# Kernel tuning notes

Measured on AMD Instinct MI355X. Metric: run time of the kernel, lower is better.

Reference implementation:

```python
import jax, jax.numpy as jnp
import numpy as np

BATCH, SEQ = 2, 4096
IN_FEATURES = 4096
OUT_FEATURES = 4096
BLOCK = 64                      # oft_block_size (bs)
RANK = IN_FEATURES // BLOCK     # number of diagonal blocks (r)


def setup_inputs() -> dict:
    key = jax.random.key(0)
    k1, k2, k3, k4 = jax.random.split(key, 4)
    x = jax.random.normal(k1, (BATCH, SEQ, IN_FEATURES), dtype=jnp.float32)
    # OFT adapter parameters: one (bs x bs) generator per block
    oft_r = jax.random.normal(k2, (RANK, BLOCK, BLOCK), dtype=jnp.float32) * 0.02
    # Dequantized GPTQ weight (out_features x in_features) + bias
    W = jax.random.normal(k3, (OUT_FEATURES, IN_FEATURES), dtype=jnp.float32) * 0.02
    b = jax.random.normal(k4, (OUT_FEATURES,), dtype=jnp.float32)
    return {"x": x, "oft_r": oft_r, "W": W, "b": b}


def _cayley_batch(data):
    # data: [r, bs, bs].  Q = (I - skew) @ (I + skew)^{-1}  (torch.linalg.solve left=False)
    bs = data.shape[-1]
    skew = 0.5 * (data - jnp.swapaxes(data, -1, -2))
    I = jnp.eye(bs, dtype=data.dtype)
    A = I + skew   # [r, bs, bs]
    B = I - skew
    # Solve Q A = B  ->  A^T Q^T = B^T
    Qt = jnp.linalg.solve(jnp.swapaxes(A, -1, -2), jnp.swapaxes(B, -1, -2))
    return jnp.swapaxes(Qt, -1, -2)


def reference(x, oft_r, W, b):
    rank, bs, _ = oft_r.shape
    # oft_rotation starts as identity; single active adapter -> rotation = Cayley(oft_r)
    oft_rotation = _cayley_batch(oft_r)            # [rank, bs, bs]
    batch_dims = x.shape[:-1]
    x_reshaped = x.reshape(*batch_dims, rank, bs)  # [..., r, k]
    x_rot = jnp.einsum('...rk,rkc->...rc', x_reshaped, oft_rotation)
    x_rot = x_rot.reshape(*batch_dims, rank * bs)  # [..., in_features]
    # quant_linear_module (dequantized): y = x_rot @ W^T + b
    return jnp.einsum('bsi,oi->bso', x_rot, W) + b
```

## Files before the change

### kernel.cpp

```cpp
#include <hip/hip_runtime.h>
#include <hip/hip_bf16.h>
#include <stdint.h>


typedef __bf16 bf16;
typedef __attribute__((ext_vector_type(4))) __bf16 bf16x4;
typedef __attribute__((ext_vector_type(8))) __bf16 bf16x8;
typedef __attribute__((ext_vector_type(4))) float f32x4;

__device__ __forceinline__ bf16 f2bf(float f) {
  unsigned u = __builtin_bit_cast(unsigned, f);
  u += 0x7fffu + ((u >> 16) & 1u);
  unsigned short h = (unsigned short)(u >> 16);
  return __builtin_bit_cast(bf16, h);
}

__global__ __launch_bounds__(256) void cayley_kernel(const float* __restrict__ oft_r,
                                                     float* __restrict__ Qxt) {
  __shared__ float St[64][68];
  __shared__ float Ta[64][65];
  __shared__ float Tb[64][65];
  const int tid = threadIdx.x;
  const int r = blockIdx.x;
  const float* D = oft_r + (size_t)r * 4096;

  for (int idx = tid; idx < 4096; idx += 256) {
    int i = idx >> 6, j = idx & 63;
    float s = 0.5f * (D[i * 64 + j] - D[j * 64 + i]);
    St[j][i] = s;
    Ta[i][j] = (i == j ? 1.0f : 0.0f) - s;
  }
  __syncthreads();

  const int j = tid & 63;
  const int w = tid >> 6;
  float (*Tin)[65] = Ta;
  float (*Tout)[65] = Tb;

  for (int it = 0; it < 5; ++it) {
    float out[16];
#pragma unroll
    for (int m = 0; m < 16; ++m) out[m] = ((w * 16 + m) == j ? 1.0f : 0.0f);
    for (int c = 0; c < 64; ++c) {
      float tc = Tin[c][j];
      f32x4 s0 = *reinterpret_cast<const f32x4*>(&St[c][w * 16]);
      f32x4 s1 = *reinterpret_cast<const f32x4*>(&St[c][w * 16 + 4]);
      f32x4 s2 = *reinterpret_cast<const f32x4*>(&St[c][w * 16 + 8]);
      f32x4 s3 = *reinterpret_cast<const f32x4*>(&St[c][w * 16 + 12]);
#pragma unroll
      for (int q = 0; q < 4; ++q) {
        out[q]      -= s0[q] * tc;
        out[4 + q]  -= s1[q] * tc;
        out[8 + q]  -= s2[q] * tc;
        out[12 + q] -= s3[q] * tc;
      }
    }
#pragma unroll
    for (int m = 0; m < 16; ++m) Tout[w * 16 + m][j] = out[m];
    __syncthreads();
    float (*tmp)[65] = Tin; Tin = Tout; Tout = tmp;
  }
  {
    float out[16];
#pragma unroll
    for (int m = 0; m < 16; ++m) out[m] = Tin[w * 16 + m][j];
    for (int c = 0; c < 64; ++c) {
      float tc = Tin[c][j];
      f32x4 s0 = *reinterpret_cast<const f32x4*>(&St[c][w * 16]);
      f32x4 s1 = *reinterpret_cast<const f32x4*>(&St[c][w * 16 + 4]);
      f32x4 s2 = *reinterpret_cast<const f32x4*>(&St[c][w * 16 + 8]);
      f32x4 s3 = *reinterpret_cast<const f32x4*>(&St[c][w * 16 + 12]);
#pragma unroll
      for (int q = 0; q < 4; ++q) {
        out[q]      -= s0[q] * tc;
        out[4 + q]  -= s1[q] * tc;
        out[8 + q]  -= s2[q] * tc;
        out[12 + q] -= s3[q] * tc;
      }
    }
#pragma unroll
    for (int m = 0; m < 16; ++m) Qxt[(size_t)r * 4096 + (w * 16 + m) * 64 + j] = out[m];
  }
}

__global__ __launch_bounds__(256) void fold_w_kernel(const float* __restrict__ W,
                                                     const float* __restrict__ Qxt,
                                                     bf16* __restrict__ Wp) {
  __shared__ bf16 Wb[128 * 64];
  __shared__ bf16 Xt[64 * 64];
  const int tid = threadIdx.x;
  const int lane = tid & 63;
  const int wave = tid >> 6;
  const int o0 = blockIdx.x * 128;
  const int r = blockIdx.y;
  const int fr = lane & 15;
  const int kg = lane >> 4;

#pragma unroll
  for (int i = 0; i < 8; ++i) {
    int c = i * 256 + tid;
    int row = c >> 4, c4 = c & 15;
    f32x4 v = *reinterpret_cast<const f32x4*>(W + (size_t)(o0 + row) * 4096 + r * 64 + c4 * 4);
    bf16x4 o; o[0] = f2bf(v[0]); o[1] = f2bf(v[1]); o[2] = f2bf(v[2]); o[3] = f2bf(v[3]);
    *reinterpret_cast<bf16x4*>(&Wb[row * 64 + c4 * 4]) = o;
  }
#pragma unroll
  for (int i = 0; i < 4; ++i) {
    int c = i * 256 + tid;
    int row = c >> 4, c4 = c & 15;
    f32x4 v = *reinterpret_cast<const f32x4*>(Qxt + (size_t)r * 4096 + row * 64 + c4 * 4);
    bf16x4 o; o[0] = f2bf(v[0]); o[1] = f2bf(v[1]); o[2] = f2bf(v[2]); o[3] = f2bf(v[3]);
    *reinterpret_cast<bf16x4*>(&Xt[row * 64 + c4 * 4]) = o;
  }
  __syncthreads();

  const int wm = wave * 32;
  f32x4 acc[2][4];
#pragma unroll
  for (int mi = 0; mi < 2; ++mi)
#pragma unroll
    for (int ni = 0; ni < 4; ++ni) acc[mi][ni] = (f32x4){0.f, 0.f, 0.f, 0.f};

#pragma unroll
  for (int kk = 0; kk < 64; kk += 32) {
    bf16x8 af[2], bx[4];
#pragma unroll
    for (int mi = 0; mi < 2; ++mi)
      af[mi] = *reinterpret_cast<const bf16x8*>(&Wb[(wm + mi * 16 + fr) * 64 + kk + kg * 8]);
#pragma unroll
    for (int ni = 0; ni < 4; ++ni)
      bx[ni] = *reinterpret_cast<const bf16x8*>(&Xt[(ni * 16 + fr) * 64 + kk + kg * 8]);
#pragma unroll
    for (int mi = 0; mi < 2; ++mi)
#pragma unroll
      for (int ni = 0; ni < 4; ++ni)
        acc[mi][ni] = __builtin_amdgcn_mfma_f32_16x16x32_bf16(af[mi], bx[ni], acc[mi][ni], 0, 0, 0);
  }

#pragma unroll
  for (int mi = 0; mi < 2; ++mi)
#pragma unroll
    for (int ni = 0; ni < 4; ++ni)
#pragma unroll
      for (int q = 0; q < 4; ++q) {
        int row = o0 + wm + mi * 16 + kg * 4 + q;
        int col = ni * 16 + fr;
        Wp[(size_t)row * 4096 + r * 64 + col] = f2bf(acc[mi][ni][q]);
      }
}

__global__ __launch_bounds__(256) void cast_x_kernel(const float* __restrict__ x,
                                                     bf16* __restrict__ xb, long n) {
  long i0 = ((long)blockIdx.x * 256 + threadIdx.x) * 8;
  long stride = (long)gridDim.x * 256 * 8;
  for (long i = i0; i < n; i += stride) {
    f32x4 a = *reinterpret_cast<const f32x4*>(x + i);
    f32x4 b = *reinterpret_cast<const f32x4*>(x + i + 4);
    bf16x8 o;
    o[0] = f2bf(a[0]); o[1] = f2bf(a[1]); o[2] = f2bf(a[2]); o[3] = f2bf(a[3]);
    o[4] = f2bf(b[0]); o[5] = f2bf(b[1]); o[6] = f2bf(b[2]); o[7] = f2bf(b[3]);
    *reinterpret_cast<bf16x8*>(xb + i) = o;
  }
}


#define GLDS16(g, l) __builtin_amdgcn_global_load_lds( \
    (const __attribute__((address_space(1))) unsigned int*)(g), \
    (__attribute__((address_space(3))) unsigned int*)(l), 16, 0, 0)

#define VMCNT4 asm volatile("s_waitcnt vmcnt(4)" ::: "memory")
#define VMCNT0 asm volatile("s_waitcnt vmcnt(0)" ::: "memory")
#define BARRIER() do { asm volatile("" ::: "memory"); \
  __builtin_amdgcn_s_barrier(); asm volatile("" ::: "memory"); } while (0)

#define MFMA16(AF, BF, RB) \
  _Pragma("unroll") \
  for (int m_ = 0; m_ < 4; ++m_) \
    _Pragma("unroll") \
    for (int n_ = 0; n_ < 4; ++n_) \
      acc[RB + m_][n_] = __builtin_amdgcn_mfma_f32_16x16x32_bf16(AF[m_], BF[n_], acc[RB + m_][n_], 0, 0, 0);

#define DO_TILE(BUF, TN, PRE) do { \
     \
    _Pragma("unroll") for (int n_ = 0; n_ < 4; ++n_) Ob[n_] = LDB(BUF, 0, n_); \
    _Pragma("unroll") for (int m_ = 0; m_ < 4; ++m_) Oa[m_] = LDA(BUF, 0, m_); \
    if (PRE) STAGE(TN, BUF ^ 1, 0); \
    BARRIER(); \
    __builtin_amdgcn_s_setprio(1); MFMA16(Oa, Ob, 0) __builtin_amdgcn_s_setprio(0); \
    BARRIER(); \
     \
    _Pragma("unroll") for (int m_ = 0; m_ < 4; ++m_) Ea[m_] = LDA(BUF, 0, 4 + m_); \
    if (PRE) STAGE(TN, BUF ^ 1, 1); \
    if (PRE) { VMCNT4; } else { VMCNT0; } \
    BARRIER(); \
    __builtin_amdgcn_s_setprio(1); MFMA16(Ea, Ob, 4) __builtin_amdgcn_s_setprio(0); \
    BARRIER(); \
     \
    _Pragma("unroll") for (int n_ = 0; n_ < 4; ++n_) Eb[n_] = LDB(BUF, 1, n_); \
    _Pragma("unroll") for (int m_ = 0; m_ < 4; ++m_) Oa[m_] = LDA(BUF, 1, m_); \
    if (PRE) STAGE(TN, BUF ^ 1, 2); \
    BARRIER(); \
    __builtin_amdgcn_s_setprio(1); MFMA16(Oa, Eb, 0) __builtin_amdgcn_s_setprio(0); \
    BARRIER(); \
     \
    _Pragma("unroll") for (int m_ = 0; m_ < 4; ++m_) Ea[m_] = LDA(BUF, 1, 4 + m_); \
    if (PRE) STAGE(TN, BUF ^ 1, 3); \
    if (PRE) { VMCNT4; } else { VMCNT0; } \
    BARRIER(); \
    __builtin_amdgcn_s_setprio(1); MFMA16(Ea, Eb, 4) __builtin_amdgcn_s_setprio(0); \
    BARRIER(); \
  } while (0)

__global__ __launch_bounds__(512, 2) void gemm_kernel(const bf16* __restrict__ A,
                                                      const bf16* __restrict__ B,
                                                      const float* __restrict__ bias,
                                                      float* __restrict__ C,
                                                      int M, int N, int K) {
  __shared__ bf16 lds[65536];
  const int tid = threadIdx.x;
  const int lane = tid & 63;
  const int wave = tid >> 6;
  const int wr = wave >> 2;
  const int wc = wave & 3;
  const int fr = lane & 15;
  const int kg = lane >> 4;
  const int m0 = blockIdx.y * 256;
  const int n0 = blockIdx.x * 256;
  const int NT = K >> 6;

  f32x4 acc[8][4];
#pragma unroll
  for (int m = 0; m < 8; ++m)
#pragma unroll
    for (int n = 0; n < 4; ++n) acc[m][n] = (f32x4){0.f, 0.f, 0.f, 0.f};

  auto STAGE = [&](int t, int db, int p) {
    const int op = p & 1, ks = p >> 1;
    const bf16* src = op ? B : A;
    const int base_row = op ? n0 : m0;
    const int ldsb = db * 32768 + op * 16384 + ks * 8192;
#pragma unroll
    for (int i = 0; i < 2; ++i) {
      int c = i * 512 + tid;
      int row = c >> 2, cc = c & 3;
      const bf16* g = src + (size_t)(base_row + row) * K + t * 64 + ks * 32
                      + ((cc ^ ((row >> 1) & 3)) << 3);
      GLDS16(g, &lds[ldsb + ((i * 512 + wave * 64) << 3)]);
    }
  };
  auto LDA = [&](int buf, int ks, int mi) -> bf16x8 {
    int row = wr * 128 + mi * 16 + fr;
    return *reinterpret_cast<const bf16x8*>(
        &lds[buf * 32768 + ks * 8192 + row * 32 + ((kg ^ ((row >> 1) & 3)) << 3)]);
  };
  auto LDB = [&](int buf, int ks, int ni) -> bf16x8 {
    int row = wc * 64 + ni * 16 + fr;
    return *reinterpret_cast<const bf16x8*>(
        &lds[buf * 32768 + 16384 + ks * 8192 + row * 32 + ((kg ^ ((row >> 1) & 3)) << 3)]);
  };

#pragma unroll
  for (int p = 0; p < 4; ++p) STAGE(0, 0, p);
  VMCNT4;
  BARRIER();

  bf16x8 Oa[4], Ob[4], Ea[4], Eb[4];
  for (int t = 0; t < NT; t += 2) {
    DO_TILE(0, t + 1, true);
    DO_TILE(1, t + 2, (t + 2) < NT);
  }

#pragma unroll
  for (int n = 0; n < 4; ++n) {
    int col = n0 + wc * 64 + n * 16 + fr;
    float bv = bias[col];
#pragma unroll
    for (int m = 0; m < 8; ++m) {
      int row0 = m0 + wr * 128 + m * 16 + kg * 4;
#pragma unroll
      for (int q = 0; q < 4; ++q)
        C[(size_t)(row0 + q) * N + col] = acc[m][n][q] + bv;
    }
  }
}

extern "C" void kernel_launch(void* const* d_in, const int* in_sizes, int n_in,
                              void* d_out, int out_size, void* d_ws, size_t ws_size,
                              hipStream_t stream) {
  const float* x     = (const float*)d_in[0];
  const float* oft_r = (const float*)d_in[1];
  const float* W     = (const float*)d_in[2];
  const float* b     = (const float*)d_in[3];
  float* y = (float*)d_out;

  char* ws = (char*)d_ws;
  float* Qxt = (float*)ws;
  bf16*  Wp  = (bf16*)(ws + (1u << 20));
  bf16*  xb  = (bf16*)(ws + (1u << 20) + (32u << 20));

  cayley_kernel<<<64, 256, 0, stream>>>(oft_r, Qxt);
  dim3 fg(32, 64);
  fold_w_kernel<<<fg, 256, 0, stream>>>(W, Qxt, Wp);
  cast_x_kernel<<<2048, 256, 0, stream>>>(x, xb, 33554432L);
  dim3 gg(4096 / 256, 8192 / 256);
  gemm_kernel<<<gg, 512, 0, stream>>>(xb, Wp, b, y, 8192, 4096, 4096);
}
```

Measured before the change: 341.3 us.

## Fuse fp32-to-bf16 activation cast into GEMM A-tile loading

Removes the separate cast kernel and has the GEMM load fp32 activations into registers, convert them to bf16 and write them into swizzled LDS. B tiles still use direct global-to-LDS loads. This drops the extra pass that wrote and re-read a bf16 copy of x. In exchange, the GEMM reads twice the bytes per A tile and uses more registers. The pipeline's wait counts are also more complex.

New measurement: 917.8 us. 2.69x slower.

```diff
diff --git a/kernel.cpp b/kernel.cpp
--- a/kernel.cpp
+++ b/kernel.cpp
@@ -149,27 +149,15 @@
       }
 }
 
-__global__ __launch_bounds__(256) void cast_x_kernel(const float* __restrict__ x,
-                                                     bf16* __restrict__ xb, long n) {
-  long i0 = ((long)blockIdx.x * 256 + threadIdx.x) * 8;
-  long stride = (long)gridDim.x * 256 * 8;
-  for (long i = i0; i < n; i += stride) {
-    f32x4 a = *reinterpret_cast<const f32x4*>(x + i);
-    f32x4 b = *reinterpret_cast<const f32x4*>(x + i + 4);
-    bf16x8 o;
-    o[0] = f2bf(a[0]); o[1] = f2bf(a[1]); o[2] = f2bf(a[2]); o[3] = f2bf(a[3]);
-    o[4] = f2bf(b[0]); o[5] = f2bf(b[1]); o[6] = f2bf(b[2]); o[7] = f2bf(b[3]);
-    *reinterpret_cast<bf16x8*>(xb + i) = o;
-  }
-}
-
 
 #define GLDS16(g, l) __builtin_amdgcn_global_load_lds( \
     (const __attribute__((address_space(1))) unsigned int*)(g), \
     (__attribute__((address_space(3))) unsigned int*)(l), 16, 0, 0)
 
-#define VMCNT4 asm volatile("s_waitcnt vmcnt(4)" ::: "memory")
+#define VMCNT6 asm volatile("s_waitcnt vmcnt(6)" ::: "memory")
+#define VMCNT2 asm volatile("s_waitcnt vmcnt(2)" ::: "memory")
 #define VMCNT0 asm volatile("s_waitcnt vmcnt(0)" ::: "memory")
+#define LGKMD  asm volatile("s_waitcnt lgkmcnt(0)" ::: "memory")
 #define BARRIER() do { asm volatile("" ::: "memory"); \
   __builtin_amdgcn_s_barrier(); asm volatile("" ::: "memory"); } while (0)
 
@@ -184,34 +172,42 @@
      \
     _Pragma("unroll") for (int n_ = 0; n_ < 4; ++n_) Ob[n_] = LDB(BUF, 0, n_); \
     _Pragma("unroll") for (int m_ = 0; m_ < 4; ++m_) Oa[m_] = LDA(BUF, 0, m_); \
-    if (PRE) STAGE(TN, BUF ^ 1, 0); \
+    if (PRE) { La0 = A_LD(TN, 0, 0); La1 = A_LD(TN, 0, 1); \
+               La2 = A_LD(TN, 0, 2); La3 = A_LD(TN, 0, 3); } \
     BARRIER(); \
     __builtin_amdgcn_s_setprio(1); MFMA16(Oa, Ob, 0) __builtin_amdgcn_s_setprio(0); \
     BARRIER(); \
      \
     _Pragma("unroll") for (int m_ = 0; m_ < 4; ++m_) Ea[m_] = LDA(BUF, 0, 4 + m_); \
-    if (PRE) STAGE(TN, BUF ^ 1, 1); \
-    if (PRE) { VMCNT4; } else { VMCNT0; } \
+    if (PRE) STAGE_B(TN, BUF ^ 1, 0); \
+    if (PRE) { VMCNT6; } else { VMCNT0; } \
     BARRIER(); \
     __builtin_amdgcn_s_setprio(1); MFMA16(Ea, Ob, 4) __builtin_amdgcn_s_setprio(0); \
     BARRIER(); \
      \
     _Pragma("unroll") for (int n_ = 0; n_ < 4; ++n_) Eb[n_] = LDB(BUF, 1, n_); \
     _Pragma("unroll") for (int m_ = 0; m_ < 4; ++m_) Oa[m_] = LDA(BUF, 1, m_); \
-    if (PRE) STAGE(TN, BUF ^ 1, 2); \
+    if (PRE) { Lb0 = A_LD(TN, 1, 0); Lb1 = A_LD(TN, 1, 1); \
+               Lb2 = A_LD(TN, 1, 2); Lb3 = A_LD(TN, 1, 3); \
+               A_WR(BUF ^ 1, 0, 0, La0); A_WR(BUF ^ 1, 0, 1, La1); \
+               A_WR(BUF ^ 1, 0, 2, La2); A_WR(BUF ^ 1, 0, 3, La3); \
+               LGKMD; } \
     BARRIER(); \
     __builtin_amdgcn_s_setprio(1); MFMA16(Oa, Eb, 0) __builtin_amdgcn_s_setprio(0); \
     BARRIER(); \
      \
     _Pragma("unroll") for (int m_ = 0; m_ < 4; ++m_) Ea[m_] = LDA(BUF, 1, 4 + m_); \
-    if (PRE) STAGE(TN, BUF ^ 1, 3); \
-    if (PRE) { VMCNT4; } else { VMCNT0; } \
+    if (PRE) STAGE_B(TN, BUF ^ 1, 1); \
+    if (PRE) { VMCNT6; } else { VMCNT0; } \
+    if (PRE) { A_WR(BUF ^ 1, 1, 0, Lb0); A_WR(BUF ^ 1, 1, 1, Lb1); \
+               A_WR(BUF ^ 1, 1, 2, Lb2); A_WR(BUF ^ 1, 1, 3, Lb3); \
+               LGKMD; } \
     BARRIER(); \
     __builtin_amdgcn_s_setprio(1); MFMA16(Ea, Eb, 4) __builtin_amdgcn_s_setprio(0); \
     BARRIER(); \
   } while (0)
 
-__global__ __launch_bounds__(512, 2) void gemm_kernel(const bf16* __restrict__ A,
+__global__ __launch_bounds__(512, 2) void gemm_kernel(const float* __restrict__ X,
                                                       const bf16* __restrict__ B,
                                                       const float* __restrict__ bias,
                                                       float* __restrict__ C,
@@ -234,19 +230,29 @@
 #pragma unroll
     for (int n = 0; n < 4; ++n) acc[m][n] = (f32x4){0.f, 0.f, 0.f, 0.f};
 
-  auto STAGE = [&](int t, int db, int p) {
-    const int op = p & 1, ks = p >> 1;
-    const bf16* src = op ? B : A;
-    const int base_row = op ? n0 : m0;
-    const int ldsb = db * 32768 + op * 16384 + ks * 8192;
+  auto STAGE_B = [&](int t, int db, int ks) {
+    const int ldsb = db * 32768 + 16384 + ks * 8192;
 #pragma unroll
     for (int i = 0; i < 2; ++i) {
       int c = i * 512 + tid;
       int row = c >> 2, cc = c & 3;
-      const bf16* g = src + (size_t)(base_row + row) * K + t * 64 + ks * 32
+      const bf16* g = B + (size_t)(n0 + row) * K + t * 64 + ks * 32
                       + ((cc ^ ((row >> 1) & 3)) << 3);
       GLDS16(g, &lds[ldsb + ((i * 512 + wave * 64) << 3)]);
     }
+  };
+  auto A_LD = [&](int t, int ks, int i) -> f32x4 {
+    int c = i * 512 + tid;
+    int row = c >> 3, f4 = c & 7;
+    return *reinterpret_cast<const f32x4*>(X + (size_t)(m0 + row) * K + t * 64 + ks * 32 + f4 * 4);
+  };
+  auto A_WR = [&](int db, int ks, int i, f32x4 v) {
+    int c = i * 512 + tid;
+    int row = c >> 3, f4 = c & 7;
+    int cc16 = f4 >> 1, half = f4 & 1;
+    bf16x4 o; o[0] = f2bf(v[0]); o[1] = f2bf(v[1]); o[2] = f2bf(v[2]); o[3] = f2bf(v[3]);
+    *reinterpret_cast<bf16x4*>(
+        &lds[db * 32768 + ks * 8192 + row * 32 + ((cc16 ^ ((row >> 1) & 3)) << 3) + half * 4]) = o;
   };
   auto LDA = [&](int buf, int ks, int mi) -> bf16x8 {
     int row = wr * 128 + mi * 16 + fr;
@@ -259,9 +265,16 @@
         &lds[buf * 32768 + 16384 + ks * 8192 + row * 32 + ((kg ^ ((row >> 1) & 3)) << 3)]);
   };
 
-#pragma unroll
-  for (int p = 0; p < 4; ++p) STAGE(0, 0, p);
-  VMCNT4;
+  f32x4 La0, La1, La2, La3, Lb0, Lb1, Lb2, Lb3;
+
+  La0 = A_LD(0, 0, 0); La1 = A_LD(0, 0, 1); La2 = A_LD(0, 0, 2); La3 = A_LD(0, 0, 3);
+  Lb0 = A_LD(0, 1, 0); Lb1 = A_LD(0, 1, 1); Lb2 = A_LD(0, 1, 2); Lb3 = A_LD(0, 1, 3);
+  STAGE_B(0, 0, 0);
+  STAGE_B(0, 0, 1);
+  A_WR(0, 0, 0, La0); A_WR(0, 0, 1, La1); A_WR(0, 0, 2, La2); A_WR(0, 0, 3, La3);
+  A_WR(0, 1, 0, Lb0); A_WR(0, 1, 1, Lb1); A_WR(0, 1, 2, Lb2); A_WR(0, 1, 3, Lb3);
+  VMCNT2;
+  LGKMD;
   BARRIER();
 
   bf16x8 Oa[4], Ob[4], Ea[4], Eb[4];
@@ -296,12 +309,10 @@
   char* ws = (char*)d_ws;
   float* Qxt = (float*)ws;
   bf16*  Wp  = (bf16*)(ws + (1u << 20));
-  bf16*  xb  = (bf16*)(ws + (1u << 20) + (32u << 20));
 
   cayley_kernel<<<64, 256, 0, stream>>>(oft_r, Qxt);
   dim3 fg(32, 64);
   fold_w_kernel<<<fg, 256, 0, stream>>>(W, Qxt, Wp);
-  cast_x_kernel<<<2048, 256, 0, stream>>>(x, xb, 33554432L);
   dim3 gg(4096 / 256, 8192 / 256);
-  gemm_kernel<<<gg, 512, 0, stream>>>(xb, Wp, b, y, 8192, 4096, 4096);
-}
+  gemm_kernel<<<gg, 512, 0, stream>>>(x, Wp, b, y, 8192, 4096, 4096);
+}
```
